# Performance work log

Measured on AMD Instinct MI355X. Metric: run time of the kernel, lower is better.

## Reference

```python
import jax, jax.numpy as jnp
import numpy as np

EPS = 1e-5
N_HEADS = 4
N_GROUPS = 32


def group_norm(x, gamma, beta, num_groups):
    # x: (B, C, H, W)
    B, C, H, W = x.shape
    xg = x.reshape(B, num_groups, (C // num_groups) * H * W)
    mean = xg.mean(axis=2, keepdims=True)
    var = xg.var(axis=2, keepdims=True)
    xn = ((xg - mean) * jax.lax.rsqrt(var + EPS)).reshape(B, C, H, W)
    return xn * gamma[None, :, None, None] + beta[None, :, None, None]


def conv1x1(x, W, b=None):
    # 1x1 conv == channel-mixing matmul: (O,C) x (B,C,H,W) -> (B,O,H,W)
    y = jnp.einsum('oc,bchw->bohw', W, x)
    if b is not None:
        y = y + b[None, :, None, None]
    return y


def setup_inputs() -> dict:
    key = jax.random.key(0)
    ks = jax.random.split(key, 8)
    B, Cq, Cc, H, W = 2, 128, 128, 64, 64
    x = jax.random.normal(ks[0], (B, Cq, H, W), dtype=jnp.float32)
    context = jax.random.normal(ks[1], (B, Cc, H, W), dtype=jnp.float32)
    sq = Cq ** -0.5
    sc = Cc ** -0.5
    return {
        'x': x,
        'context': context,
        'gq': jnp.ones((Cq,), jnp.float32),
        'bq': jnp.zeros((Cq,), jnp.float32),
        'gctx': jnp.ones((Cc,), jnp.float32),
        'bctx': jnp.zeros((Cc,), jnp.float32),
        'Wq': jax.random.normal(ks[2], (Cq, Cq), jnp.float32) * sq,
        'Wk': jax.random.normal(ks[3], (Cq, Cc), jnp.float32) * sc,
        'Wv': jax.random.normal(ks[4], (Cq, Cc), jnp.float32) * sc,
        'Wout': jax.random.normal(ks[5], (Cq, Cq), jnp.float32) * 0.02,
        'bout': jnp.zeros((Cq,), jnp.float32),
        'alpha': jnp.asarray(1.0, jnp.float32),
    }


def reference(x, context, gq, bq, gctx, bctx, Wq, Wk, Wv, Wout, bout, alpha):
    B, C, H, W = x.shape
    hd = C // N_HEADS
    # QKV projections (GroupNorm + 1x1 conv); note v uses raw context (no norm)
    q = conv1x1(group_norm(x, gq, bq, N_GROUPS), Wq)
    k = conv1x1(group_norm(context, gctx, bctx, N_GROUPS), Wk)
    v = conv1x1(context, Wv)
    q = q.reshape(B, N_HEADS, hd, H * W)
    k = k.reshape(B, N_HEADS, hd, H * W)
    v = v.reshape(B, N_HEADS, hd, H * W)
    scale = jnp.asarray(hd ** 0.5, x.dtype)
    attn = jnp.einsum('bncd,bnce->bnde', q, k) / scale  # (B, nH, HW, HW)
    attn = jax.nn.softmax(attn, axis=-1)
    out = jnp.einsum('bnde,bnce->bncd', attn, v).reshape(B, C, H, W)
    return x + alpha * conv1x1(out, Wout, bout)
```

## Files before the change

kernel.cpp:

```cpp
#include <hip/hip_runtime.h>
#include <hip/hip_bf16.h>
#include <math.h>

#define L 4096
#define C 128
#define NH 4
#define HD 32
#define KS 4
#define EPSV 1e-5f

typedef short bf16x8 __attribute__((ext_vector_type(8)));
typedef float f32x4 __attribute__((ext_vector_type(4)));

static __device__ __forceinline__ unsigned pack2bf(float a, float b) {
    __hip_bfloat162 h = __float22bfloat162_rn(make_float2(a, b));
    unsigned u; __builtin_memcpy(&u, &h, 4); return u;
}
static __device__ __forceinline__ float bf_lo(unsigned u) {
    unsigned v = u << 16; float f; __builtin_memcpy(&f, &v, 4); return f;
}
static __device__ __forceinline__ float bf_hi(unsigned u) {
    unsigned v = u & 0xffff0000u; float f; __builtin_memcpy(&f, &v, 4); return f;
}

__global__ __launch_bounds__(256) void gn_stats_kernel(
    const float* __restrict__ x, const float* __restrict__ ctx,
    float* __restrict__ stats)
{
    int bid = blockIdx.x;
    int t = threadIdx.x;
    const float* in = (bid < 64) ? x : ctx;
    int rem = bid & 63;
    const float4* p = (const float4*)(in + (size_t)rem * 16384);
    float s = 0.f, s2 = 0.f;
    for (int i = t; i < 4096; i += 256) {
        float4 v = p[i];
        s  += v.x + v.y + v.z + v.w;
        s2 += v.x*v.x + v.y*v.y + v.z*v.z + v.w*v.w;
    }
    #pragma unroll
    for (int m = 32; m >= 1; m >>= 1) {
        s  += __shfl_xor(s, m);
        s2 += __shfl_xor(s2, m);
    }
    __shared__ float wsum[4][2];
    int w = t >> 6;
    if ((t & 63) == 0) { wsum[w][0] = s; wsum[w][1] = s2; }
    __syncthreads();
    if (t == 0) {
        float S = wsum[0][0] + wsum[1][0] + wsum[2][0] + wsum[3][0];
        float S2 = wsum[0][1] + wsum[1][1] + wsum[2][1] + wsum[3][1];
        float mean = S * (1.f / 16384.f);
        float var = S2 * (1.f / 16384.f) - mean * mean;
        stats[bid * 2]     = mean;
        stats[bid * 2 + 1] = rsqrtf(var + EPSV);
    }
}

__global__ __launch_bounds__(256) void proj_kernel(
    const float* __restrict__ x, const float* __restrict__ ctx,
    const float* __restrict__ gq, const float* __restrict__ bq,
    const float* __restrict__ gctx, const float* __restrict__ bctx,
    const float* __restrict__ stats,
    const float* __restrict__ Wq, const float* __restrict__ Wk,
    const float* __restrict__ Wv,
    unsigned short* __restrict__ Qt, unsigned short* __restrict__ Kt,
    unsigned short* __restrict__ Vsw)
{
    int t = threadIdx.x;
    int w = t >> 6, lane = t & 63, n16 = lane & 15, quad = lane >> 4;
    int dtile = blockIdx.x * 32;
    int b = blockIdx.y, z = blockIdx.z;

    const float* in; const float* Wm; const float* gamma; const float* beta;
    int sel = 1, donorm = 1; float oscale = 1.f;
    if (z == 0)      { in = x;   Wm = Wq; gamma = gq;   beta = bq;   sel = 0;
                       oscale = 0.17677669529663689f * 1.4426950408889634f; }
    else if (z == 1) { in = ctx; Wm = Wk; gamma = gctx; beta = bctx; }
    else             { in = ctx; Wm = Wv; gamma = 0;    beta = 0;    donorm = 0; }

    __shared__ __attribute__((aligned(16))) unsigned short Xs[32 * 136];

    {
        int c0 = (t >> 3) * 4, d4 = (t & 7) * 4;
        const float* inb = in + (size_t)b * (C * L);
        float vv[4][4];
        #pragma unroll
        for (int j = 0; j < 4; j++) {
            int c = c0 + j;
            float sc = 1.f, sh = 0.f;
            if (donorm) {
                int sidx = (sel * 64 + b * 32 + (c >> 2)) * 2;
                float mean = stats[sidx], inv = stats[sidx + 1];
                sc = inv * gamma[c];
                sh = beta[c] - mean * sc;
            }
            float4 v = *(const float4*)(inb + (size_t)c * L + dtile + d4);
            vv[j][0] = v.x * sc + sh; vv[j][1] = v.y * sc + sh;
            vv[j][2] = v.z * sc + sh; vv[j][3] = v.w * sc + sh;
        }
        #pragma unroll
        for (int i = 0; i < 4; i++) {
            uint2 pk;
            pk.x = pack2bf(vv[0][i], vv[1][i]);
            pk.y = pack2bf(vv[2][i], vv[3][i]);
            *(uint2*)&Xs[(d4 + i) * 136 + c0] = pk;
        }
    }

    bf16x8 wa[2][4];
    #pragma unroll
    for (int os2 = 0; os2 < 2; os2++) {
        const float* wr = Wm + (size_t)(((w + os2 * 4) * 16) + n16) * C + quad * 8;
        #pragma unroll
        for (int kk = 0; kk < 4; kk++) {
            float4 a  = *(const float4*)(wr + kk * 32);
            float4 b2 = *(const float4*)(wr + kk * 32 + 4);
            unsigned u4[4] = { pack2bf(a.x, a.y),  pack2bf(a.z, a.w),
                               pack2bf(b2.x, b2.y), pack2bf(b2.z, b2.w) };
            __builtin_memcpy(&wa[os2][kk], u4, 16);
        }
    }
    __syncthreads();

    f32x4 zero = {0.f, 0.f, 0.f, 0.f};
    f32x4 acc[2][2];
    acc[0][0] = zero; acc[0][1] = zero; acc[1][0] = zero; acc[1][1] = zero;
    #pragma unroll
    for (int kk = 0; kk < 4; kk++) {
        #pragma unroll
        for (int dg = 0; dg < 2; dg++) {
            bf16x8 xb;
            uint4 u = *(const uint4*)&Xs[(dg * 16 + n16) * 136 + kk * 32 + quad * 8];
            __builtin_memcpy(&xb, &u, 16);
            acc[0][dg] = __builtin_amdgcn_mfma_f32_16x16x32_bf16(wa[0][kk], xb, acc[0][dg], 0, 0, 0);
            acc[1][dg] = __builtin_amdgcn_mfma_f32_16x16x32_bf16(wa[1][kk], xb, acc[1][dg], 0, 0, 0);
        }
    }

    #pragma unroll
    for (int os2 = 0; os2 < 2; os2++) {
        int o = ((w + os2 * 4) * 16) + quad * 4;
        int h = o >> 5, c32 = o & 31;
        #pragma unroll
        for (int dg = 0; dg < 2; dg++) {
            int d = dtile + dg * 16 + n16;
            if (z < 2) {
                unsigned short* outp = (z == 0) ? Qt : Kt;
                uint2 pk;
                pk.x = pack2bf(acc[os2][dg][0] * oscale, acc[os2][dg][1] * oscale);
                pk.y = pack2bf(acc[os2][dg][2] * oscale, acc[os2][dg][3] * oscale);
                *(uint2*)(outp + ((size_t)(b * NH + h) * L + d) * HD + c32) = pk;
            } else {
                unsigned short* vb = Vsw + (size_t)(b * NH + h) * (L * HD)
                                   + (size_t)(d >> 3) * 256 + (d & 7);
                #pragma unroll
                for (int r = 0; r < 4; r++) {
                    __hip_bfloat16 hv = __float2bfloat16(acc[os2][dg][r]);
                    unsigned short us; __builtin_memcpy(&us, &hv, 2);
                    vb[(c32 + r) * 8] = us;
                }
            }
        }
    }
}

__global__ __launch_bounds__(256, 4) void flash_kernel(
    const unsigned short* __restrict__ Qt, const unsigned short* __restrict__ Kt,
    const unsigned short* __restrict__ Vsw, unsigned short* __restrict__ Po,
    float* __restrict__ Pl)
{
    __shared__ __attribute__((aligned(16))) unsigned short Ps[4 * 2 * 16 * 72];

    int t = threadIdx.x;
    int w = t >> 6, lane = t & 63;
    int n16 = lane & 15, quad = lane >> 4;
    int bh = blockIdx.x;
    int qbase = blockIdx.y * 128 + w * 32;
    int ks = blockIdx.z;
    size_t hb = (size_t)bh * (L * HD);

    bf16x8 qf[2];
    #pragma unroll
    for (int sp = 0; sp < 2; sp++) {
        uint4 u = *(const uint4*)(Qt + hb + (size_t)(qbase + sp * 16 + n16) * HD + quad * 8);
        __builtin_memcpy(&qf[sp], &u, 16);
    }

    const unsigned short* kfp = Kt + hb + (size_t)n16 * HD + quad * 8;
    const unsigned short* vfp = Vsw + hb + quad * 256 + n16 * 8;

    int e0 = ks * (L / KS);

    bf16x8 ka[2][4];
    #pragma unroll
    for (int et = 0; et < 4; et++) {
        uint4 u = *(const uint4*)(kfp + (size_t)(e0 + et * 16) * HD);
        __builtin_memcpy(&ka[0][et], &u, 16);
    }

    float lsum[2] = {0.f, 0.f};
    f32x4 zero = {0.f, 0.f, 0.f, 0.f};
    f32x4 oacc[2][2];
    oacc[0][0] = zero; oacc[0][1] = zero; oacc[1][0] = zero; oacc[1][1] = zero;

    #pragma unroll 2
    for (int kt = 0; kt < L / KS / 64; kt++) {
        int cur = kt & 1, nxt = cur ^ 1;
        int ecur = e0 + kt * 64;
        #pragma unroll
        for (int et = 0; et < 4; et++) {
            uint4 u = *(const uint4*)(kfp + (size_t)(ecur + 64 + et * 16) * HD);
            __builtin_memcpy(&ka[nxt][et], &u, 16);
        }
        bf16x8 va[4];
        #pragma unroll
        for (int es = 0; es < 2; es++)
            #pragma unroll
            for (int f = 0; f < 2; f++) {
                uint4 u = *(const uint4*)(vfp + (size_t)(ecur + es * 32) * 32 + f * 128);
                __builtin_memcpy(&va[es * 2 + f], &u, 16);
            }

        #pragma unroll
        for (int sp = 0; sp < 2; sp++) {
            f32x4 s[4];
            #pragma unroll
            for (int et = 0; et < 4; et++)
                s[et] = __builtin_amdgcn_mfma_f32_16x16x32_bf16(ka[cur][et], qf[sp], zero, 0, 0, 0);
            float p[4][4];
            #pragma unroll
            for (int et = 0; et < 4; et++)
                #pragma unroll
                for (int r = 0; r < 4; r++) {
                    p[et][r] = __builtin_amdgcn_exp2f(s[et][r]);
                    lsum[sp] += p[et][r];
                }
            unsigned short* pw = Ps + ((w * 2 + sp) * 1152) + n16 * 72;
            #pragma unroll
            for (int et = 0; et < 4; et++) {
                uint2 pk;
                pk.x = pack2bf(p[et][0], p[et][1]);
                pk.y = pack2bf(p[et][2], p[et][3]);
                *(uint2*)(pw + et * 16 + quad * 4) = pk;
            }
        }

        #pragma unroll
        for (int sp = 0; sp < 2; sp++) {
            unsigned short* pw = Ps + ((w * 2 + sp) * 1152) + n16 * 72;
            #pragma unroll
            for (int es = 0; es < 2; es++) {
                bf16x8 pf;
                uint4 u = *(const uint4*)(pw + es * 32 + quad * 8);
                __builtin_memcpy(&pf, &u, 16);
                oacc[sp][0] = __builtin_amdgcn_mfma_f32_16x16x32_bf16(va[es * 2 + 0], pf, oacc[sp][0], 0, 0, 0);
                oacc[sp][1] = __builtin_amdgcn_mfma_f32_16x16x32_bf16(va[es * 2 + 1], pf, oacc[sp][1], 0, 0, 0);
            }
        }
    }

    #pragma unroll
    for (int sp = 0; sp < 2; sp++) {
        float ls = lsum[sp];
        ls += __shfl_xor(ls, 16);
        ls += __shfl_xor(ls, 32);
        int dq = qbase + sp * 16 + n16;
        unsigned short* po = Po + ((size_t)(bh * KS + ks) * L + dq) * 32;
        uint2 pk0, pk1;
        pk0.x = pack2bf(oacc[sp][0][0], oacc[sp][0][1]);
        pk0.y = pack2bf(oacc[sp][0][2], oacc[sp][0][3]);
        pk1.x = pack2bf(oacc[sp][1][0], oacc[sp][1][1]);
        pk1.y = pack2bf(oacc[sp][1][2], oacc[sp][1][3]);
        *(uint2*)(po + quad * 4)      = pk0;
        *(uint2*)(po + 16 + quad * 4) = pk1;
        if (quad == 0)
            Pl[(size_t)(bh * KS + ks) * L + dq] = ls;
    }
}

__global__ __launch_bounds__(256) void final_kernel(
    const unsigned short* __restrict__ Po, const float* __restrict__ Pl,
    const float* __restrict__ x, const float* __restrict__ Wout,
    const float* __restrict__ bout, const float* __restrict__ alpha,
    float* __restrict__ out)
{
    int t = threadIdx.x;
    int w = t >> 6, lane = t & 63, n16 = lane & 15, quad = lane >> 4;
    int dtile = blockIdx.x * 16;
    int b = blockIdx.y;

    __shared__ __attribute__((aligned(16))) float Ot[128 * 20];
    unsigned short* Xs = (unsigned short*)Ot;

    {
        int d_l = t >> 4, c0 = (t & 15) * 8;
        int dq = dtile + d_l;
        int bh = b * NH + (c0 >> 5);
        int c32 = c0 & 31;
        float l = 0.f;
        float o8[8] = {0.f, 0.f, 0.f, 0.f, 0.f, 0.f, 0.f, 0.f};
        #pragma unroll
        for (int ks = 0; ks < KS; ks++) {
            size_t base = (size_t)(bh * KS + ks) * L + dq;
            l += Pl[base];
            uint4 u = *(const uint4*)(Po + base * 32 + c32);
            o8[0] += bf_lo(u.x); o8[1] += bf_hi(u.x);
            o8[2] += bf_lo(u.y); o8[3] += bf_hi(u.y);
            o8[4] += bf_lo(u.z); o8[5] += bf_hi(u.z);
            o8[6] += bf_lo(u.w); o8[7] += bf_hi(u.w);
        }
        float rl = 1.f / l;
        uint4 pk;
        pk.x = pack2bf(o8[0] * rl, o8[1] * rl);
        pk.y = pack2bf(o8[2] * rl, o8[3] * rl);
        pk.z = pack2bf(o8[4] * rl, o8[5] * rl);
        pk.w = pack2bf(o8[6] * rl, o8[7] * rl);
        *(uint4*)&Xs[d_l * 136 + c0] = pk;
    }

    bf16x8 wa[2][4];
    #pragma unroll
    for (int os2 = 0; os2 < 2; os2++) {
        const float* wr = Wout + (size_t)(((w + os2 * 4) * 16) + n16) * C + quad * 8;
        #pragma unroll
        for (int kk = 0; kk < 4; kk++) {
            float4 a  = *(const float4*)(wr + kk * 32);
            float4 b2 = *(const float4*)(wr + kk * 32 + 4);
            unsigned u4[4] = { pack2bf(a.x, a.y),  pack2bf(a.z, a.w),
                               pack2bf(b2.x, b2.y), pack2bf(b2.z, b2.w) };
            __builtin_memcpy(&wa[os2][kk], u4, 16);
        }
    }
    __syncthreads();

    f32x4 zero = {0.f, 0.f, 0.f, 0.f};
    f32x4 acc[2];
    acc[0] = zero; acc[1] = zero;
    #pragma unroll
    for (int kk = 0; kk < 4; kk++) {
        bf16x8 xb;
        uint4 u = *(const uint4*)&Xs[n16 * 136 + kk * 32 + quad * 8];
        __builtin_memcpy(&xb, &u, 16);
        acc[0] = __builtin_amdgcn_mfma_f32_16x16x32_bf16(wa[0][kk], xb, acc[0], 0, 0, 0);
        acc[1] = __builtin_amdgcn_mfma_f32_16x16x32_bf16(wa[1][kk], xb, acc[1], 0, 0, 0);
    }
    __syncthreads();

    #pragma unroll
    for (int os2 = 0; os2 < 2; os2++) {
        int o = ((w + os2 * 4) * 16) + quad * 4;
        #pragma unroll
        for (int r = 0; r < 4; r++)
            Ot[(o + r) * 20 + n16] = acc[os2][r];
    }
    __syncthreads();

    float al = alpha[0];
    int o = t >> 1, dh = (t & 1) * 8;
    float bo = bout[o];
    const float* xb2 = x + ((size_t)b * C + o) * L + dtile + dh;
    float* ob = out + ((size_t)b * C + o) * L + dtile + dh;
    #pragma unroll
    for (int jj = 0; jj < 2; jj++) {
        float4 a  = *(const float4*)&Ot[o * 20 + dh + jj * 4];
        float4 xv = *(const float4*)(xb2 + jj * 4);
        float4 r;
        r.x = xv.x + al * (a.x + bo);
        r.y = xv.y + al * (a.y + bo);
        r.z = xv.z + al * (a.z + bo);
        r.w = xv.w + al * (a.w + bo);
        *(float4*)(ob + jj * 4) = r;
    }
}

extern "C" void kernel_launch(void* const* d_in, const int* in_sizes, int n_in,
                              void* d_out, int out_size, void* d_ws, size_t ws_size,
                              hipStream_t stream) {
    const float* x     = (const float*)d_in[0];
    const float* ctx   = (const float*)d_in[1];
    const float* gq    = (const float*)d_in[2];
    const float* bq    = (const float*)d_in[3];
    const float* gctx  = (const float*)d_in[4];
    const float* bctx  = (const float*)d_in[5];
    const float* Wq    = (const float*)d_in[6];
    const float* Wk    = (const float*)d_in[7];
    const float* Wv    = (const float*)d_in[8];
    const float* Wout  = (const float*)d_in[9];
    const float* bout  = (const float*)d_in[10];
    const float* alpha = (const float*)d_in[11];
    float* out = (float*)d_out;

    char* ws = (char*)d_ws;
    unsigned short* Qt  = (unsigned short*)(ws);
    unsigned short* Kt  = (unsigned short*)(ws + 2097152);
    unsigned short* Vsw = (unsigned short*)(ws + 4194304);
    unsigned short* Po  = (unsigned short*)(ws + 6291456);
    float*          Pl  = (float*)(ws + 14680064);
    float*          stats = (float*)(ws + 15204352);

    gn_stats_kernel<<<128, 256, 0, stream>>>(x, ctx, stats);
    proj_kernel<<<dim3(128, 2, 3), 256, 0, stream>>>(x, ctx, gq, bq, gctx, bctx,
                                                     stats, Wq, Wk, Wv, Qt, Kt, Vsw);
    flash_kernel<<<dim3(8, 32, KS), 256, 0, stream>>>(Qt, Kt, Vsw, Po, Pl);
    final_kernel<<<dim3(256, 2), 256, 0, stream>>>(Po, Pl, x, Wout, bout, alpha, out);
}
```

Before: 135.6 us.

## Use bit-trick exp2 and MFMA ones-row for softmax denominators, unroll GN stats

Replaces the hardware exp2 in the attention inner loop with a Schraudolph-style bit-manipulation approximation built from an fma and an int conversion. The per-thread row-sum of probabilities is replaced by an extra MFMA that multiplies the packed bf16 P tile by a vector of ones, moving the denominator onto the matrix unit and removing the shuffles. The group-norm stats loop is manually unrolled. The fast exp2 is a coarse piecewise-linear approximation, which risks accuracy, and the extra MFMA adds matrix work in the inner loop.

```diff
diff --git a/kernel.cpp b/kernel.cpp
--- a/kernel.cpp
+++ b/kernel.cpp
@@ -21,6 +21,12 @@
 }
 static __device__ __forceinline__ float bf_hi(unsigned u) {
     unsigned v = u & 0xffff0000u; float f; __builtin_memcpy(&f, &v, 4); return f;
+}
+static __device__ __forceinline__ float fast_exp2(float x) {
+    float t = fmaf(x, 8388608.f, 1064992212.f);
+    int i = (int)t;
+    float r; __builtin_memcpy(&r, &i, 4);
+    return r;
 }
 
 __global__ __launch_bounds__(256) void gn_stats_kernel(
@@ -33,8 +39,27 @@
     int rem = bid & 63;
     const float4* p = (const float4*)(in + (size_t)rem * 16384);
     float s = 0.f, s2 = 0.f;
-    for (int i = t; i < 4096; i += 256) {
-        float4 v = p[i];
+    #pragma unroll
+    for (int rr = 0; rr < 4; rr++) {
+        float4 v = p[t + rr * 256];
+        s  += v.x + v.y + v.z + v.w;
+        s2 += v.x*v.x + v.y*v.y + v.z*v.z + v.w*v.w;
+    }
+    #pragma unroll
+    for (int rr = 0; rr < 4; rr++) {
+        float4 v = p[t + 1024 + rr * 256];
+        s  += v.x + v.y + v.z + v.w;
+        s2 += v.x*v.x + v.y*v.y + v.z*v.z + v.w*v.w;
+    }
+    #pragma unroll
+    for (int rr = 0; rr < 4; rr++) {
+        float4 v = p[t + 2048 + rr * 256];
+        s  += v.x + v.y + v.z + v.w;
+        s2 += v.x*v.x + v.y*v.y + v.z*v.z + v.w*v.w;
+    }
+    #pragma unroll
+    for (int rr = 0; rr < 4; rr++) {
+        float4 v = p[t + 3072 + rr * 256];
         s  += v.x + v.y + v.z + v.w;
         s2 += v.x*v.x + v.y*v.y + v.z*v.z + v.w*v.w;
     }
@@ -187,6 +212,10 @@
         __builtin_memcpy(&qf[sp], &u, 16);
     }
 
+    bf16x8 onesf;
+    #pragma unroll
+    for (int j = 0; j < 8; j++) onesf[j] = (short)0x3F80;
+
     const unsigned short* kfp = Kt + hb + (size_t)n16 * HD + quad * 8;
     const unsigned short* vfp = Vsw + hb + quad * 256 + n16 * 8;
 
@@ -199,10 +228,10 @@
         __builtin_memcpy(&ka[0][et], &u, 16);
     }
 
-    float lsum[2] = {0.f, 0.f};
     f32x4 zero = {0.f, 0.f, 0.f, 0.f};
-    f32x4 oacc[2][2];
+    f32x4 oacc[2][2], lacc[2];
     oacc[0][0] = zero; oacc[0][1] = zero; oacc[1][0] = zero; oacc[1][1] = zero;
+    lacc[0] = zero; lacc[1] = zero;
 
     #pragma unroll 2
     for (int kt = 0; kt < L / KS / 64; kt++) {
@@ -228,20 +257,12 @@
             #pragma unroll
             for (int et = 0; et < 4; et++)
                 s[et] = __builtin_amdgcn_mfma_f32_16x16x32_bf16(ka[cur][et], qf[sp], zero, 0, 0, 0);
-            float p[4][4];
-            #pragma unroll
-            for (int et = 0; et < 4; et++)
-                #pragma unroll
-                for (int r = 0; r < 4; r++) {
-                    p[et][r] = __builtin_amdgcn_exp2f(s[et][r]);
-                    lsum[sp] += p[et][r];
-                }
             unsigned short* pw = Ps + ((w * 2 + sp) * 1152) + n16 * 72;
             #pragma unroll
             for (int et = 0; et < 4; et++) {
                 uint2 pk;
-                pk.x = pack2bf(p[et][0], p[et][1]);
-                pk.y = pack2bf(p[et][2], p[et][3]);
+                pk.x = pack2bf(fast_exp2(s[et][0]), fast_exp2(s[et][1]));
+                pk.y = pack2bf(fast_exp2(s[et][2]), fast_exp2(s[et][3]));
                 *(uint2*)(pw + et * 16 + quad * 4) = pk;
             }
         }
@@ -256,15 +277,13 @@
                 __builtin_memcpy(&pf, &u, 16);
                 oacc[sp][0] = __builtin_amdgcn_mfma_f32_16x16x32_bf16(va[es * 2 + 0], pf, oacc[sp][0], 0, 0, 0);
                 oacc[sp][1] = __builtin_amdgcn_mfma_f32_16x16x32_bf16(va[es * 2 + 1], pf, oacc[sp][1], 0, 0, 0);
+                lacc[sp]    = __builtin_amdgcn_mfma_f32_16x16x32_bf16(onesf, pf, lacc[sp], 0, 0, 0);
             }
         }
     }
 
     #pragma unroll
     for (int sp = 0; sp < 2; sp++) {
-        float ls = lsum[sp];
-        ls += __shfl_xor(ls, 16);
-        ls += __shfl_xor(ls, 32);
         int dq = qbase + sp * 16 + n16;
         unsigned short* po = Po + ((size_t)(bh * KS + ks) * L + dq) * 32;
         uint2 pk0, pk1;
@@ -275,7 +294,7 @@
         *(uint2*)(po + quad * 4)      = pk0;
         *(uint2*)(po + 16 + quad * 4) = pk1;
         if (quad == 0)
-            Pl[(size_t)(bh * KS + ks) * L + dq] = ls;
+            Pl[(size_t)(bh * KS + ks) * L + dq] = lacc[sp][0];
     }
 }
 
```

Result: faster. 128.1 us (-5.5%).
